# Kernel tuning notes

Measured on AMD Instinct MI355X. Metric: run time of the kernel, lower is better.

Reference implementation:

```python
import jax, jax.numpy as jnp
import numpy as np

BN_EPS = 1e-5

def _batchnorm(h, gamma, beta):
    # PyTorch BatchNorm1d in training mode: biased batch statistics over dim 0
    mu = jnp.mean(h, axis=0)
    var = jnp.mean((h - mu) ** 2, axis=0)
    return (h - mu) * jax.lax.rsqrt(var + BN_EPS) * gamma + beta


def setup_inputs() -> dict:
    key = jax.random.key(0)
    ks = jax.random.split(key, 8)
    N, E, D = 50000, 800000, 128
    x = jax.random.normal(ks[0], (N, D), dtype=jnp.float32)
    edge_index = jax.random.randint(ks[1], (2, E), 0, N, dtype=jnp.int64)
    s1 = 1.0 / np.sqrt(D)
    W1 = jax.random.uniform(ks[2], (D, D), jnp.float32, -s1, s1)
    b1 = jax.random.uniform(ks[3], (D,), jnp.float32, -s1, s1)
    W2 = jax.random.uniform(ks[4], (D, D), jnp.float32, -s1, s1)
    b2 = jax.random.uniform(ks[5], (D,), jnp.float32, -s1, s1)
    g1 = jnp.ones((D,), jnp.float32); beta1 = jnp.zeros((D,), jnp.float32)
    g2 = jnp.ones((D,), jnp.float32); beta2 = jnp.zeros((D,), jnp.float32)
    eps = jnp.array([0.1], jnp.float32)
    return {"x": x, "edge_index": edge_index, "eps": eps,
            "W1": W1, "b1": b1, "g1": g1, "beta1": beta1,
            "W2": W2, "b2": b2, "g2": g2, "beta2": beta2}


def reference(x, edge_index, eps, W1, b1, g1, beta1, W2, b2, g2, beta2):
    src, dst = edge_index[0], edge_index[1]
    N = x.shape[0]
    # gather by src, scatter-add to dst
    aggr = jax.ops.segment_sum(x[src], dst, num_segments=N)
    out = (1.0 + eps) * x + aggr  # eps broadcast (shape [1])
    h = jax.nn.relu(_batchnorm(out @ W1 + b1, g1, beta1))
    h = jax.nn.relu(_batchnorm(h @ W2 + b2, g2, beta2))
    return h
```

## Files before the change

kernel.cpp:

```cpp
#include <hip/hip_runtime.h>

#define D 128
#define FB 4096
#define GCAP 512

typedef __attribute__((ext_vector_type(8))) short short8;
typedef __attribute__((ext_vector_type(4))) float f32x4;

static __device__ __forceinline__ unsigned short f2bf(float f) {
    union { float f; unsigned u; } v; v.f = f;
    unsigned r = v.u + 0x7FFF + ((v.u >> 16) & 1);
    return (unsigned short)(r >> 16);
}

static __device__ __forceinline__ float2 bfpair2f(unsigned p) {
    union { unsigned u; float f; } a, b;
    a.u = (p & 0xFFFFu) << 16;
    b.u = p & 0xFFFF0000u;
    return make_float2(a.f, b.f);
}

__global__ __launch_bounds__(256) void prep_kernel(
    const float4* __restrict__ x4, uint2* __restrict__ xh, int xtotal,
    const float* __restrict__ W1, const float* __restrict__ W2,
    unsigned short* __restrict__ Wf1, unsigned short* __restrict__ Wf2,
    float* __restrict__ stats, int* __restrict__ bucketCount,
    unsigned short* __restrict__ zrow, int xblocks)
{
    if (blockIdx.x < (unsigned)xblocks) {
        int i = blockIdx.x * 256 + threadIdx.x;
        if (i >= xtotal) return;
        float4 v = x4[i];
        uint2 o;
        o.x = (unsigned)f2bf(v.x) | ((unsigned)f2bf(v.y) << 16);
        o.y = (unsigned)f2bf(v.z) | ((unsigned)f2bf(v.w) << 16);
        xh[i] = o;
    } else if (blockIdx.x < (unsigned)(xblocks + 128)) {
        int idx = (blockIdx.x - xblocks) * 256 + threadIdx.x;
        const float* W = (idx < 16384) ? W1 : W2;
        unsigned short* Wf = (idx < 16384) ? Wf1 : Wf2;
        int e = idx & 16383;
        int j = e & 7, lane = (e >> 3) & 63, ckk = e >> 9;
        int ct = ckk & 7, kk = ckk >> 3;
        int k = kk * 32 + (lane >> 4) * 8 + j;
        int n = ct * 16 + (lane & 15);
        Wf[e] = f2bf(W[k * 128 + n]);
    } else {
        int t = threadIdx.x;
        stats[t] = 0.f; stats[t + 256] = 0.f;
        bucketCount[t] = 0; bucketCount[t + 256] = 0;
        if (t < 128) zrow[t] = 0;
    }
}

__global__ __launch_bounds__(256) void bucket_hist_kernel(
    const int* __restrict__ ei, int E, int NB, int* __restrict__ bucketCount)
{
    __shared__ int hist[512];
    int tid = threadIdx.x;
    for (int i = tid; i < NB; i += 256) hist[i] = 0;
    __syncthreads();
    int b0 = blockIdx.x * FB;
    int lim = min(FB, E - b0);
    for (int i = tid; i < lim; i += 256)
        atomicAdd(&hist[ei[E + b0 + i] >> 7], 1);
    __syncthreads();
    for (int i = tid; i < NB; i += 256)
        if (hist[i]) atomicAdd(&bucketCount[i], hist[i]);
}

__global__ __launch_bounds__(512) void bucket_scan_kernel(
    const int* __restrict__ bucketCount, int NB, int E,
    int* __restrict__ bucketBase, int* __restrict__ bucketCursor)
{
    __shared__ int sm[512];
    int tid = threadIdx.x;
    int v = (tid < NB) ? bucketCount[tid] : 0;
    sm[tid] = v;
    __syncthreads();
    #pragma unroll
    for (int off = 1; off < 512; off <<= 1) {
        int u = (tid >= off) ? sm[tid - off] : 0;
        __syncthreads();
        sm[tid] += u;
        __syncthreads();
    }
    if (tid < NB) {
        int ex = sm[tid] - v;
        bucketBase[tid] = ex;
        bucketCursor[tid] = ex;
    }
    if (tid == 0) bucketBase[NB] = E;
}

__global__ __launch_bounds__(256) void bucket_fill_kernel(
    const int* __restrict__ ei, int E, int NB,
    int* __restrict__ bucketCursor, unsigned* __restrict__ rec)
{
    __shared__ int hist[512], base[512];
    int tid = threadIdx.x;
    int b0 = blockIdx.x * FB;
    for (int i = tid; i < NB; i += 256) hist[i] = 0;
    __syncthreads();
    int lim = min(FB, E - b0);
    for (int i = tid; i < lim; i += 256)
        atomicAdd(&hist[ei[E + b0 + i] >> 7], 1);
    __syncthreads();
    for (int i = tid; i < NB; i += 256) {
        int c = hist[i];
        base[i] = c ? atomicAdd(&bucketCursor[i], c) : 0;
        hist[i] = 0;
    }
    __syncthreads();
    for (int i = tid; i < lim; i += 256) {
        int e = b0 + i;
        int dst = ei[E + e], src = ei[e];
        int bk = dst >> 7;
        int r = atomicAdd(&hist[bk], 1);
        rec[base[bk] + r] = ((unsigned)src << 7) | (unsigned)(dst & 127);
    }
}

__global__ __launch_bounds__(256) void bucket_gather_kernel(
    const unsigned* __restrict__ xh, const unsigned* __restrict__ rec,
    const int* __restrict__ bucketBase, const float* __restrict__ epsp,
    unsigned* __restrict__ h0, int N, int zrow)
{
    int bk = blockIdx.x >> 3;
    int sub = blockIdx.x & 7;
    int tid = threadIdx.x;
    int d0 = (bk << 7) + (sub << 4);

    __shared__ int cnts[16], rnk[16], offs[17];
    __shared__ int slist[GCAP];

    if (tid < 16) { cnts[tid] = 0; rnk[tid] = 0; }
    __syncthreads();

    int lo = bucketBase[bk], hi = bucketBase[bk + 1];
    for (int i = lo + tid; i < hi; i += 256) {
        unsigned r = rec[i];
        int dl = r & 127;
        if ((dl >> 4) == sub) atomicAdd(&cnts[dl & 15], 1);
    }
    __syncthreads();
    if (tid == 0) {
        int run = 0;
        #pragma unroll
        for (int i = 0; i < 16; ++i) { offs[i] = run; run += cnts[i]; }
        offs[16] = run;
    }
    __syncthreads();
    for (int i = lo + tid; i < hi; i += 256) {
        unsigned r = rec[i];
        int dl = r & 127;
        if ((dl >> 4) == sub) {
            int d4 = dl & 15;
            int rk = atomicAdd(&rnk[d4], 1);
            int pos = offs[d4] + rk;
            if (pos < GCAP) slist[pos] = (int)(r >> 7);
        }
    }
    __syncthreads();

    int wv = tid >> 6, lane = tid & 63;
    float epsv = 1.0f + __ldg(epsp);

    int dloc = wv * 4;
    int dA = d0 + dloc, dB = dA + 1, dC = dA + 2, dD = dA + 3;
    int vA = (dA < N), vB = (dB < N), vC = (dC < N), vD = (dD < N);

    int iA = offs[dloc + 0], eA = offs[dloc + 1];
    int iB = offs[dloc + 1], eB = offs[dloc + 2];
    int iC = offs[dloc + 2], eC = offs[dloc + 3];
    int iD = offs[dloc + 3], eD = offs[dloc + 4];
    if (iA > GCAP) iA = GCAP;  if (eA > GCAP) eA = GCAP;
    if (iB > GCAP) iB = GCAP;  if (eB > GCAP) eB = GCAP;
    if (iC > GCAP) iC = GCAP;  if (eC > GCAP) eC = GCAP;
    if (iD > GCAP) iD = GCAP;  if (eD > GCAP) eD = GCAP;
    if (!vA) { iA = 0; eA = 0; }
    if (!vB) { iB = 0; eB = 0; }
    if (!vC) { iC = 0; eC = 0; }
    if (!vD) { iD = 0; eD = 0; }

    float2 xvA = bfpair2f(xh[(size_t)(vA ? dA : 0) * 64 + lane]);
    float2 xvB = bfpair2f(xh[(size_t)(vB ? dB : 0) * 64 + lane]);
    float2 xvC = bfpair2f(xh[(size_t)(vC ? dC : 0) * 64 + lane]);
    float2 xvD = bfpair2f(xh[(size_t)(vD ? dD : 0) * 64 + lane]);
    float axA = epsv * xvA.x, ayA = epsv * xvA.y;
    float axB = epsv * xvB.x, ayB = epsv * xvB.y;
    float axC = epsv * xvC.x, ayC = epsv * xvC.y;
    float axD = epsv * xvD.x, ayD = epsv * xvD.y;

    int rA = eA - iA, rB = eB - iB, rC = eC - iC, rD = eD - iD;
    int iters = max(max(rA, rB), max(rC, rD));
    for (int it = 0; it < iters; it += 8) {
        unsigned pA[8], pB[8], pC[8], pD[8];
        #pragma unroll
        for (int k = 0; k < 8; ++k) {
            int idxA = (iA + k < eA) ? slist[iA + k] : zrow;
            int idxB = (iB + k < eB) ? slist[iB + k] : zrow;
            int idxC = (iC + k < eC) ? slist[iC + k] : zrow;
            int idxD = (iD + k < eD) ? slist[iD + k] : zrow;
            pA[k] = xh[(size_t)idxA * 64 + lane];
            pB[k] = xh[(size_t)idxB * 64 + lane];
            pC[k] = xh[(size_t)idxC * 64 + lane];
            pD[k] = xh[(size_t)idxD * 64 + lane];
        }
        #pragma unroll
        for (int k = 0; k < 8; ++k) {
            float2 a = bfpair2f(pA[k]);
            float2 b = bfpair2f(pB[k]);
            float2 c = bfpair2f(pC[k]);
            float2 d = bfpair2f(pD[k]);
            axA += a.x; ayA += a.y;
            axB += b.x; ayB += b.y;
            axC += c.x; ayC += c.y;
            axD += d.x; ayD += d.y;
        }
        iA += 8; iB += 8; iC += 8; iD += 8;
    }
    if (vA) h0[(size_t)dA * 64 + lane] =
        (unsigned)f2bf(axA) | ((unsigned)f2bf(ayA) << 16);
    if (vB) h0[(size_t)dB * 64 + lane] =
        (unsigned)f2bf(axB) | ((unsigned)f2bf(ayB) << 16);
    if (vC) h0[(size_t)dC * 64 + lane] =
        (unsigned)f2bf(axC) | ((unsigned)f2bf(ayC) << 16);
    if (vD) h0[(size_t)dD * 64 + lane] =
        (unsigned)f2bf(axD) | ((unsigned)f2bf(ayD) << 16);
}

static __device__ __forceinline__ short8 bn_relu_pack(
    const unsigned short* arow, int c, const float* scf, const float* shf)
{
    uint4 rw = *(const uint4*)(arow + c);
    float2 p0 = bfpair2f(rw.x), p1 = bfpair2f(rw.y);
    float2 p2 = bfpair2f(rw.z), p3 = bfpair2f(rw.w);
    p0.x = fmaxf(fmaf(p0.x, scf[c + 0], shf[c + 0]), 0.f);
    p0.y = fmaxf(fmaf(p0.y, scf[c + 1], shf[c + 1]), 0.f);
    p1.x = fmaxf(fmaf(p1.x, scf[c + 2], shf[c + 2]), 0.f);
    p1.y = fmaxf(fmaf(p1.y, scf[c + 3], shf[c + 3]), 0.f);
    p2.x = fmaxf(fmaf(p2.x, scf[c + 4], shf[c + 4]), 0.f);
    p2.y = fmaxf(fmaf(p2.y, scf[c + 5], shf[c + 5]), 0.f);
    p3.x = fmaxf(fmaf(p3.x, scf[c + 6], shf[c + 6]), 0.f);
    p3.y = fmaxf(fmaf(p3.y, scf[c + 7], shf[c + 7]), 0.f);
    short8 af;
    af[0] = (short)f2bf(p0.x); af[1] = (short)f2bf(p0.y);
    af[2] = (short)f2bf(p1.x); af[3] = (short)f2bf(p1.y);
    af[4] = (short)f2bf(p2.x); af[5] = (short)f2bf(p2.y);
    af[6] = (short)f2bf(p3.x); af[7] = (short)f2bf(p3.y);
    return af;
}

__global__ __launch_bounds__(256) void gemm_bn_mfma_kernel(
    const unsigned short* __restrict__ a_bf,
    const float* __restrict__ stat_in, const float* __restrict__ gamma,
    const float* __restrict__ beta, float invN,
    const unsigned short* __restrict__ Wf, const float* __restrict__ bias,
    unsigned short* __restrict__ zout,
    float* __restrict__ stat_sum, float* __restrict__ stat_sq,
    int N, int mode)
{
    __shared__ unsigned short Wl[16384];
    __shared__ float part[1024];
    __shared__ float scf[128], shf[128];

    int tid = threadIdx.x;
    {
        float4* dst = (float4*)Wl;
        const float4* srcp = (const float4*)Wf;
        #pragma unroll
        for (int i = 0; i < 8; ++i) dst[tid + i * 256] = srcp[tid + i * 256];
    }
    if (mode == 1 && tid < 128) {
        float mean = stat_in[tid] * invN;
        float var  = stat_in[128 + tid] * invN - mean * mean;
        float sv = gamma[tid] * rsqrtf(var + 1e-5f);
        scf[tid] = sv;
        shf[tid] = fmaf(-mean, sv, beta[tid]);
    }
    __syncthreads();

    int w = tid >> 6, lane = tid & 63, q = lane >> 4, n16 = lane & 15;
    int rowb = blockIdx.x * 128 + w * 16;
    int m0 = rowb + n16;
    int m1 = rowb + 64 + n16;
    int mc0 = (m0 < N) ? m0 : (N - 1);
    int mc1 = (m1 < N) ? m1 : (N - 1);
    const unsigned short* arow0 = a_bf + (size_t)mc0 * D;
    const unsigned short* arow1 = a_bf + (size_t)mc1 * D;

    f32x4 acc0[8], acc1[8];
    #pragma unroll
    for (int ct = 0; ct < 8; ++ct) {
        acc0[ct] = (f32x4){0.f, 0.f, 0.f, 0.f};
        acc1[ct] = (f32x4){0.f, 0.f, 0.f, 0.f};
    }

    #pragma unroll
    for (int kk = 0; kk < 4; ++kk) {
        int c = kk * 32 + q * 8;
        short8 af0, af1;
        if (mode == 0) {
            af0 = *(const short8*)(arow0 + c);
            af1 = *(const short8*)(arow1 + c);
        } else {
            af0 = bn_relu_pack(arow0, c, scf, shf);
            af1 = bn_relu_pack(arow1, c, scf, shf);
        }
        #pragma unroll
        for (int ct = 0; ct < 8; ++ct) {
            short8 bf = *(const short8*)&Wl[(((kk * 8 + ct) * 64) + lane) * 8];
            acc0[ct] = __builtin_amdgcn_mfma_f32_16x16x32_bf16(af0, bf, acc0[ct], 0, 0, 0);
            acc1[ct] = __builtin_amdgcn_mfma_f32_16x16x32_bf16(af1, bf, acc1[ct], 0, 0, 0);
        }
    }

    #pragma unroll
    for (int ct = 0; ct < 8; ++ct) {
        int col = ct * 16 + n16;
        float bv = __ldg(bias + col);
        float s = 0.f, qs = 0.f;
        #pragma unroll
        for (int reg = 0; reg < 4; ++reg) {
            int row = rowb + q * 4 + reg;
            float v = acc0[ct][reg] + bv;
            if (row < N) {
                zout[(size_t)row * D + col] = f2bf(v);
                s += v;
                qs = fmaf(v, v, qs);
            }
        }
        #pragma unroll
        for (int reg = 0; reg < 4; ++reg) {
            int row = rowb + 64 + q * 4 + reg;
            float v = acc1[ct][reg] + bv;
            if (row < N) {
                zout[(size_t)row * D + col] = f2bf(v);
                s += v;
                qs = fmaf(v, v, qs);
            }
        }
        s  += __shfl_xor(s, 16, 64);
        s  += __shfl_xor(s, 32, 64);
        qs += __shfl_xor(qs, 16, 64);
        qs += __shfl_xor(qs, 32, 64);
        if (lane < 16) {
            part[w * 128 + col] = s;
            part[512 + w * 128 + col] = qs;
        }
    }
    __syncthreads();

    if (tid < 128) {
        float s  = part[tid] + part[128 + tid] + part[256 + tid] + part[384 + tid];
        float qq = part[512 + tid] + part[640 + tid] + part[768 + tid] + part[896 + tid];
        atomicAdd(&stat_sum[tid], s);
        atomicAdd(&stat_sq[tid], qq);
    }
}

__global__ __launch_bounds__(256) void bn_relu_kernel(
    const uint2* __restrict__ z2, float4* __restrict__ out,
    const float* __restrict__ stat2, const float* __restrict__ gamma,
    const float* __restrict__ beta, float invN, int total4)
{
    __shared__ float sf[128], tf[128];
    int tid = threadIdx.x;
    if (tid < 128) {
        float mean = stat2[tid] * invN;
        float var  = stat2[128 + tid] * invN - mean * mean;
        float sv = gamma[tid] * rsqrtf(var + 1e-5f);
        sf[tid] = sv;
        tf[tid] = fmaf(-mean, sv, beta[tid]);
    }
    __syncthreads();

    int i = blockIdx.x * 256 + tid;
    if (i >= total4) return;
    uint2 zp = z2[i];
    float2 v01 = bfpair2f(zp.x);
    float2 v23 = bfpair2f(zp.y);
    int c = (i & 31) * 4;
    float4 o;
    o.x = fmaxf(fmaf(v01.x, sf[c + 0], tf[c + 0]), 0.f);
    o.y = fmaxf(fmaf(v01.y, sf[c + 1], tf[c + 1]), 0.f);
    o.z = fmaxf(fmaf(v23.x, sf[c + 2], tf[c + 2]), 0.f);
    o.w = fmaxf(fmaf(v23.y, sf[c + 3], tf[c + 3]), 0.f);
    out[i] = o;
}

extern "C" void kernel_launch(void* const* d_in, const int* in_sizes, int n_in,
                              void* d_out, int out_size, void* d_ws, size_t ws_size,
                              hipStream_t stream)
{
    const float* x   = (const float*)d_in[0];
    const int*   ei  = (const int*)d_in[1];
    const float* eps = (const float*)d_in[2];
    const float* W1  = (const float*)d_in[3];
    const float* b1  = (const float*)d_in[4];
    const float* g1  = (const float*)d_in[5];
    const float* be1 = (const float*)d_in[6];
    const float* W2  = (const float*)d_in[7];
    const float* b2  = (const float*)d_in[8];
    const float* g2  = (const float*)d_in[9];
    const float* be2 = (const float*)d_in[10];

    int N = in_sizes[0] / D;
    int E = in_sizes[1] / 2;
    size_t ND = (size_t)N * D;
    int NB = (N + 127) >> 7;

    unsigned short* xh  = (unsigned short*)d_ws;
    unsigned short* z1  = xh;
    unsigned short* region2 = xh + ND + 128;
    unsigned* rec       = (unsigned*)region2;
    unsigned short* z2  = region2;
    float* stats        = (float*)(region2 + ND);
    int* bucketCount    = (int*)(stats + 512);
    int* bucketBase     = bucketCount + 512;
    int* bucketCursor   = bucketBase + 513;
    unsigned short* Wf1 = (unsigned short*)(bucketCursor + 512);
    unsigned short* Wf2 = Wf1 + 16384;

    float* sum1 = stats + 0,   *sq1 = stats + 128;
    float* sum2 = stats + 256, *sq2 = stats + 384;
    unsigned short* h0 = (unsigned short*)d_out;

    int xtotal = N * 32;
    int xblocks = (xtotal + 255) / 256;
    prep_kernel<<<xblocks + 129, 256, 0, stream>>>(
        (const float4*)x, (uint2*)xh, xtotal, W1, W2, Wf1, Wf2,
        stats, bucketCount, xh + ND, xblocks);

    int fblocks = (E + FB - 1) / FB;
    bucket_hist_kernel<<<fblocks, 256, 0, stream>>>(ei, E, NB, bucketCount);
    bucket_scan_kernel<<<1, 512, 0, stream>>>(bucketCount, NB, E, bucketBase, bucketCursor);
    bucket_fill_kernel<<<fblocks, 256, 0, stream>>>(ei, E, NB, bucketCursor, rec);
    bucket_gather_kernel<<<NB * 8, 256, 0, stream>>>(
        (const unsigned*)xh, rec, bucketBase, eps, (unsigned*)h0, N, N);

    int gblocks = (N + 127) / 128;
    gemm_bn_mfma_kernel<<<gblocks, 256, 0, stream>>>(
        h0, nullptr, nullptr, nullptr, 0.f,
        Wf1, b1, z1, sum1, sq1, N, 0);
    gemm_bn_mfma_kernel<<<gblocks, 256, 0, stream>>>(
        z1, sum1, g1, be1, 1.0f / N,
        Wf2, b2, z2, sum2, sq2, N, 1);
    bn_relu_kernel<<<(N * 32 + 255) / 256, 256, 0, stream>>>(
        (const uint2*)z2, (float4*)d_out, sum2, g2, be2, 1.0f / N, N * 32);
}
```

Before: 222.9 us.

## Bucket edges per 16 destinations and gather rows with half-wave uint2 loads

Shrinks the edge bucket granularity from 128 to 16 destination nodes. Each gather block now reads only its own bucket, where before eight sub-blocks each rescanned a 128-node bucket. The scan becomes a two-level per-thread scan so it can cover up to 3328 buckets. The gather pads each node's source list to multiples of 8 with a zero-row sentinel and has the two wave halves load different edges as 8-byte chunks, combining them with a cross-half shuffle. In exchange the bucket histogram and fill kernels use larger shared arrays, which may lower their occupancy.

Result: slower. 229.5 us (+3.0%).

```diff
diff --git a/kernel.cpp b/kernel.cpp
--- a/kernel.cpp
+++ b/kernel.cpp
@@ -1,8 +1,10 @@
 #include <hip/hip_runtime.h>
 
 #define D 128
-#define FB 4096
+#define FB2 8192
 #define GCAP 512
+#define NBMAX 3328
+#define SCAN_PER 13
 
 typedef __attribute__((ext_vector_type(8))) short short8;
 typedef __attribute__((ext_vector_type(4))) float f32x4;
@@ -18,6 +20,35 @@
     a.u = (p & 0xFFFFu) << 16;
     b.u = p & 0xFFFF0000u;
     return make_float2(a.f, b.f);
+}
+
+static __device__ __forceinline__ void acc2(f32x4& A, uint2 p) {
+    union { unsigned u; float f; } t;
+    float f0, f1, f2, f3;
+    t.u = p.x << 16;          f0 = t.f;
+    t.u = p.x & 0xFFFF0000u;  f1 = t.f;
+    t.u = p.y << 16;          f2 = t.f;
+    t.u = p.y & 0xFFFF0000u;  f3 = t.f;
+    A[0] += f0; A[1] += f1; A[2] += f2; A[3] += f3;
+}
+
+static __device__ __forceinline__ void emit_row(
+    unsigned* h0, int d, unsigned lane8, float epsv, uint2 xv, f32x4 A)
+{
+    union { unsigned u; float f; } t;
+    float x0, x1, x2, x3;
+    t.u = xv.x << 16;          x0 = t.f;
+    t.u = xv.x & 0xFFFF0000u;  x1 = t.f;
+    t.u = xv.y << 16;          x2 = t.f;
+    t.u = xv.y & 0xFFFF0000u;  x3 = t.f;
+    float r0 = fmaf(epsv, x0, A[0]);
+    float r1 = fmaf(epsv, x1, A[1]);
+    float r2 = fmaf(epsv, x2, A[2]);
+    float r3 = fmaf(epsv, x3, A[3]);
+    uint2 o;
+    o.x = (unsigned)f2bf(r0) | ((unsigned)f2bf(r1) << 16);
+    o.y = (unsigned)f2bf(r2) | ((unsigned)f2bf(r3) << 16);
+    *(uint2*)((char*)h0 + ((unsigned)(d * 256) + lane8)) = o;
 }
 
 __global__ __launch_bounds__(256) void prep_kernel(
@@ -48,65 +79,78 @@
     } else {
         int t = threadIdx.x;
         stats[t] = 0.f; stats[t + 256] = 0.f;
-        bucketCount[t] = 0; bucketCount[t + 256] = 0;
+        for (int i = t; i < NBMAX; i += 256) bucketCount[i] = 0;
         if (t < 128) zrow[t] = 0;
     }
 }
 
 __global__ __launch_bounds__(256) void bucket_hist_kernel(
-    const int* __restrict__ ei, int E, int NB, int* __restrict__ bucketCount)
-{
-    __shared__ int hist[512];
-    int tid = threadIdx.x;
-    for (int i = tid; i < NB; i += 256) hist[i] = 0;
-    __syncthreads();
-    int b0 = blockIdx.x * FB;
-    int lim = min(FB, E - b0);
+    const int* __restrict__ ei, int E, int NB2, int* __restrict__ bucketCount)
+{
+    __shared__ int hist[NBMAX];
+    int tid = threadIdx.x;
+    for (int i = tid; i < NB2; i += 256) hist[i] = 0;
+    __syncthreads();
+    int b0 = blockIdx.x * FB2;
+    int lim = min(FB2, E - b0);
     for (int i = tid; i < lim; i += 256)
-        atomicAdd(&hist[ei[E + b0 + i] >> 7], 1);
-    __syncthreads();
-    for (int i = tid; i < NB; i += 256)
+        atomicAdd(&hist[ei[E + b0 + i] >> 4], 1);
+    __syncthreads();
+    for (int i = tid; i < NB2; i += 256)
         if (hist[i]) atomicAdd(&bucketCount[i], hist[i]);
 }
 
-__global__ __launch_bounds__(512) void bucket_scan_kernel(
-    const int* __restrict__ bucketCount, int NB, int E,
+__global__ __launch_bounds__(256) void bucket_scan_kernel(
+    const int* __restrict__ bucketCount, int NB2, int E,
     int* __restrict__ bucketBase, int* __restrict__ bucketCursor)
 {
-    __shared__ int sm[512];
-    int tid = threadIdx.x;
-    int v = (tid < NB) ? bucketCount[tid] : 0;
-    sm[tid] = v;
-    __syncthreads();
-    #pragma unroll
-    for (int off = 1; off < 512; off <<= 1) {
-        int u = (tid >= off) ? sm[tid - off] : 0;
+    __shared__ int part[256];
+    int tid = threadIdx.x;
+    int loc[SCAN_PER];
+    int s = 0;
+    #pragma unroll
+    for (int j = 0; j < SCAN_PER; ++j) {
+        int idx = tid * SCAN_PER + j;
+        int v = (idx < NB2) ? bucketCount[idx] : 0;
+        loc[j] = s;
+        s += v;
+    }
+    part[tid] = s;
+    __syncthreads();
+    #pragma unroll
+    for (int off = 1; off < 256; off <<= 1) {
+        int u = (tid >= off) ? part[tid - off] : 0;
         __syncthreads();
-        sm[tid] += u;
+        part[tid] += u;
         __syncthreads();
     }
-    if (tid < NB) {
-        int ex = sm[tid] - v;
-        bucketBase[tid] = ex;
-        bucketCursor[tid] = ex;
-    }
-    if (tid == 0) bucketBase[NB] = E;
+    int tb = (tid > 0) ? part[tid - 1] : 0;
+    #pragma unroll
+    for (int j = 0; j < SCAN_PER; ++j) {
+        int idx = tid * SCAN_PER + j;
+        if (idx < NB2) {
+            int ex = tb + loc[j];
+            bucketBase[idx] = ex;
+            bucketCursor[idx] = ex;
+        }
+    }
+    if (tid == 0) bucketBase[NB2] = E;
 }
 
 __global__ __launch_bounds__(256) void bucket_fill_kernel(
-    const int* __restrict__ ei, int E, int NB,
+    const int* __restrict__ ei, int E, int NB2,
     int* __restrict__ bucketCursor, unsigned* __restrict__ rec)
 {
-    __shared__ int hist[512], base[512];
-    int tid = threadIdx.x;
-    int b0 = blockIdx.x * FB;
-    for (int i = tid; i < NB; i += 256) hist[i] = 0;
-    __syncthreads();
-    int lim = min(FB, E - b0);
+    __shared__ int hist[NBMAX], base[NBMAX];
+    int tid = threadIdx.x;
+    int b0 = blockIdx.x * FB2;
+    for (int i = tid; i < NB2; i += 256) hist[i] = 0;
+    __syncthreads();
+    int lim = min(FB2, E - b0);
     for (int i = tid; i < lim; i += 256)
-        atomicAdd(&hist[ei[E + b0 + i] >> 7], 1);
-    __syncthreads();
-    for (int i = tid; i < NB; i += 256) {
+        atomicAdd(&hist[ei[E + b0 + i] >> 4], 1);
+    __syncthreads();
+    for (int i = tid; i < NB2; i += 256) {
         int c = hist[i];
         base[i] = c ? atomicAdd(&bucketCursor[i], c) : 0;
         hist[i] = 0;
@@ -115,119 +159,116 @@
     for (int i = tid; i < lim; i += 256) {
         int e = b0 + i;
         int dst = ei[E + e], src = ei[e];
-        int bk = dst >> 7;
+        int bk = dst >> 4;
         int r = atomicAdd(&hist[bk], 1);
-        rec[base[bk] + r] = ((unsigned)src << 7) | (unsigned)(dst & 127);
+        rec[base[bk] + r] = ((unsigned)src << 4) | (unsigned)(dst & 15);
     }
 }
 
 __global__ __launch_bounds__(256) void bucket_gather_kernel(
     const unsigned* __restrict__ xh, const unsigned* __restrict__ rec,
     const int* __restrict__ bucketBase, const float* __restrict__ epsp,
-    unsigned* __restrict__ h0, int N, int zrow)
-{
-    int bk = blockIdx.x >> 3;
-    int sub = blockIdx.x & 7;
-    int tid = threadIdx.x;
-    int d0 = (bk << 7) + (sub << 4);
+    unsigned* __restrict__ h0, int N, int zoff)
+{
+    int g = blockIdx.x;
+    int tid = threadIdx.x;
+    int d0 = g << 4;
 
     __shared__ int cnts[16], rnk[16], offs[17];
-    __shared__ int slist[GCAP];
+    __shared__ int slist[GCAP + 8];
 
     if (tid < 16) { cnts[tid] = 0; rnk[tid] = 0; }
-    __syncthreads();
-
-    int lo = bucketBase[bk], hi = bucketBase[bk + 1];
+    for (int i = tid; i < GCAP + 8; i += 256) slist[i] = zoff;
+    __syncthreads();
+
+    int lo = bucketBase[g], hi = bucketBase[g + 1];
+    for (int i = lo + tid; i < hi; i += 256)
+        atomicAdd(&cnts[rec[i] & 15], 1);
+    __syncthreads();
+    if (tid == 0) {
+        int run = 0;
+        #pragma unroll
+        for (int i = 0; i < 16; ++i) {
+            offs[i] = run;
+            run += (cnts[i] + 7) & ~7;
+            if (run > GCAP) run = GCAP;
+        }
+        offs[16] = run;
+    }
+    __syncthreads();
     for (int i = lo + tid; i < hi; i += 256) {
         unsigned r = rec[i];
-        int dl = r & 127;
-        if ((dl >> 4) == sub) atomicAdd(&cnts[dl & 15], 1);
-    }
-    __syncthreads();
-    if (tid == 0) {
-        int run = 0;
-        #pragma unroll
-        for (int i = 0; i < 16; ++i) { offs[i] = run; run += cnts[i]; }
-        offs[16] = run;
-    }
-    __syncthreads();
-    for (int i = lo + tid; i < hi; i += 256) {
-        unsigned r = rec[i];
-        int dl = r & 127;
-        if ((dl >> 4) == sub) {
-            int d4 = dl & 15;
-            int rk = atomicAdd(&rnk[d4], 1);
-            int pos = offs[d4] + rk;
-            if (pos < GCAP) slist[pos] = (int)(r >> 7);
-        }
+        int d = r & 15;
+        int rk = atomicAdd(&rnk[d], 1);
+        int pos = offs[d] + rk;
+        if (pos < offs[d + 1]) slist[pos] = (int)((r >> 4) << 8);
     }
     __syncthreads();
 
     int wv = tid >> 6, lane = tid & 63;
+    int half = lane >> 5, l5 = lane & 31;
+    unsigned lane8 = (unsigned)(l5 << 3);
     float epsv = 1.0f + __ldg(epsp);
+    const char* xc = (const char*)xh;
 
     int dloc = wv * 4;
     int dA = d0 + dloc, dB = dA + 1, dC = dA + 2, dD = dA + 3;
     int vA = (dA < N), vB = (dB < N), vC = (dC < N), vD = (dD < N);
 
-    int iA = offs[dloc + 0], eA = offs[dloc + 1];
-    int iB = offs[dloc + 1], eB = offs[dloc + 2];
-    int iC = offs[dloc + 2], eC = offs[dloc + 3];
-    int iD = offs[dloc + 3], eD = offs[dloc + 4];
-    if (iA > GCAP) iA = GCAP;  if (eA > GCAP) eA = GCAP;
-    if (iB > GCAP) iB = GCAP;  if (eB > GCAP) eB = GCAP;
-    if (iC > GCAP) iC = GCAP;  if (eC > GCAP) eC = GCAP;
-    if (iD > GCAP) iD = GCAP;  if (eD > GCAP) eD = GCAP;
-    if (!vA) { iA = 0; eA = 0; }
-    if (!vB) { iB = 0; eB = 0; }
-    if (!vC) { iC = 0; eC = 0; }
-    if (!vD) { iD = 0; eD = 0; }
-
-    float2 xvA = bfpair2f(xh[(size_t)(vA ? dA : 0) * 64 + lane]);
-    float2 xvB = bfpair2f(xh[(size_t)(vB ? dB : 0) * 64 + lane]);
-    float2 xvC = bfpair2f(xh[(size_t)(vC ? dC : 0) * 64 + lane]);
-    float2 xvD = bfpair2f(xh[(size_t)(vD ? dD : 0) * 64 + lane]);
-    float axA = epsv * xvA.x, ayA = epsv * xvA.y;
-    float axB = epsv * xvB.x, ayB = epsv * xvB.y;
-    float axC = epsv * xvC.x, ayC = epsv * xvC.y;
-    float axD = epsv * xvD.x, ayD = epsv * xvD.y;
-
-    int rA = eA - iA, rB = eB - iB, rC = eC - iC, rD = eD - iD;
-    int iters = max(max(rA, rB), max(rC, rD));
-    for (int it = 0; it < iters; it += 8) {
-        unsigned pA[8], pB[8], pC[8], pD[8];
-        #pragma unroll
-        for (int k = 0; k < 8; ++k) {
-            int idxA = (iA + k < eA) ? slist[iA + k] : zrow;
-            int idxB = (iB + k < eB) ? slist[iB + k] : zrow;
-            int idxC = (iC + k < eC) ? slist[iC + k] : zrow;
-            int idxD = (iD + k < eD) ? slist[iD + k] : zrow;
-            pA[k] = xh[(size_t)idxA * 64 + lane];
-            pB[k] = xh[(size_t)idxB * 64 + lane];
-            pC[k] = xh[(size_t)idxC * 64 + lane];
-            pD[k] = xh[(size_t)idxD * 64 + lane];
-        }
-        #pragma unroll
-        for (int k = 0; k < 8; ++k) {
-            float2 a = bfpair2f(pA[k]);
-            float2 b = bfpair2f(pB[k]);
-            float2 c = bfpair2f(pC[k]);
-            float2 d = bfpair2f(pD[k]);
-            axA += a.x; ayA += a.y;
-            axB += b.x; ayB += b.y;
-            axC += c.x; ayC += c.y;
-            axD += d.x; ayD += d.y;
-        }
-        iA += 8; iB += 8; iC += 8; iD += 8;
-    }
-    if (vA) h0[(size_t)dA * 64 + lane] =
-        (unsigned)f2bf(axA) | ((unsigned)f2bf(ayA) << 16);
-    if (vB) h0[(size_t)dB * 64 + lane] =
-        (unsigned)f2bf(axB) | ((unsigned)f2bf(ayB) << 16);
-    if (vC) h0[(size_t)dC * 64 + lane] =
-        (unsigned)f2bf(axC) | ((unsigned)f2bf(ayC) << 16);
-    if (vD) h0[(size_t)dD * 64 + lane] =
-        (unsigned)f2bf(axD) | ((unsigned)f2bf(ayD) << 16);
+    int s0 = offs[dloc + 0], s1 = offs[dloc + 1];
+    int s2 = offs[dloc + 2], s3 = offs[dloc + 3], s4 = offs[dloc + 4];
+    int nch0 = (s1 - s0) >> 3, nch1 = (s2 - s1) >> 3;
+    int nch2 = (s3 - s2) >> 3, nch3 = (s4 - s3) >> 3;
+    int iters = max(max(nch0, nch1), max(nch2, nch3));
+
+    uint2 xv0 = *(const uint2*)(xc + (unsigned)((vA ? dA : 0) * 256) + lane8);
+    uint2 xv1 = *(const uint2*)(xc + (unsigned)((vB ? dB : 0) * 256) + lane8);
+    uint2 xv2 = *(const uint2*)(xc + (unsigned)((vC ? dC : 0) * 256) + lane8);
+    uint2 xv3 = *(const uint2*)(xc + (unsigned)((vD ? dD : 0) * 256) + lane8);
+
+    f32x4 A0 = (f32x4){0.f, 0.f, 0.f, 0.f};
+    f32x4 A1 = (f32x4){0.f, 0.f, 0.f, 0.f};
+    f32x4 A2 = (f32x4){0.f, 0.f, 0.f, 0.f};
+    f32x4 A3 = (f32x4){0.f, 0.f, 0.f, 0.f};
+
+    for (int c = 0; c < iters; ++c) {
+        int b0 = (c < nch0) ? (s0 + (c << 3)) : GCAP;
+        int b1 = (c < nch1) ? (s1 + (c << 3)) : GCAP;
+        int b2 = (c < nch2) ? (s2 + (c << 3)) : GCAP;
+        int b3 = (c < nch3) ? (s3 + (c << 3)) : GCAP;
+        uint2 p0[4], p1[4], p2[4], p3[4];
+        #pragma unroll
+        for (int k = 0; k < 4; ++k) {
+            unsigned o0 = (unsigned)slist[b0 + 2 * k + half];
+            unsigned o1 = (unsigned)slist[b1 + 2 * k + half];
+            unsigned o2 = (unsigned)slist[b2 + 2 * k + half];
+            unsigned o3 = (unsigned)slist[b3 + 2 * k + half];
+            p0[k] = *(const uint2*)(xc + (o0 + lane8));
+            p1[k] = *(const uint2*)(xc + (o1 + lane8));
+            p2[k] = *(const uint2*)(xc + (o2 + lane8));
+            p3[k] = *(const uint2*)(xc + (o3 + lane8));
+        }
+        #pragma unroll
+        for (int k = 0; k < 4; ++k) {
+            acc2(A0, p0[k]); acc2(A1, p1[k]);
+            acc2(A2, p2[k]); acc2(A3, p3[k]);
+        }
+    }
+
+    #pragma unroll
+    for (int r = 0; r < 4; ++r) {
+        A0[r] += __shfl_xor(A0[r], 32, 64);
+        A1[r] += __shfl_xor(A1[r], 32, 64);
+        A2[r] += __shfl_xor(A2[r], 32, 64);
+        A3[r] += __shfl_xor(A3[r], 32, 64);
+    }
+
+    if (half == 0) {
+        if (vA) emit_row(h0, dA, lane8, epsv, xv0, A0);
+        if (vB) emit_row(h0, dB, lane8, epsv, xv1, A1);
+        if (vC) emit_row(h0, dC, lane8, epsv, xv2, A2);
+        if (vD) emit_row(h0, dD, lane8, epsv, xv3, A3);
+    }
 }
 
 static __device__ __forceinline__ short8 bn_relu_pack(
@@ -409,18 +450,18 @@
     int N = in_sizes[0] / D;
     int E = in_sizes[1] / 2;
     size_t ND = (size_t)N * D;
-    int NB = (N + 127) >> 7;
+    int NB2 = (N + 15) >> 4;
 
     unsigned short* xh  = (unsigned short*)d_ws;
     unsigned short* z1  = xh;
     unsigned short* region2 = xh + ND + 128;
     unsigned* rec       = (unsigned*)region2;
     unsigned short* z2  = region2;
+    int* bucketCount    = (int*)((char*)region2 + (4 << 20));
+    int* bucketBase     = bucketCount + NBMAX;
+    int* bucketCursor   = bucketBase + NBMAX + 1;
     float* stats        = (float*)(region2 + ND);
-    int* bucketCount    = (int*)(stats + 512);
-    int* bucketBase     = bucketCount + 512;
-    int* bucketCursor   = bucketBase + 513;
-    unsigned short* Wf1 = (unsigned short*)(bucketCursor + 512);
+    unsigned short* Wf1 = (unsigned short*)(stats + 512);
     unsigned short* Wf2 = Wf1 + 16384;
 
     float* sum1 = stats + 0,   *sq1 = stats + 128;
@@ -433,12 +474,12 @@
         (const float4*)x, (uint2*)xh, xtotal, W1, W2, Wf1, Wf2,
         stats, bucketCount, xh + ND, xblocks);
 
-    int fblocks = (E + FB - 1) / FB;
-    bucket_hist_kernel<<<fblocks, 256, 0, stream>>>(ei, E, NB, bucketCount);
-    bucket_scan_kernel<<<1, 512, 0, stream>>>(bucketCount, NB, E, bucketBase, bucketCursor);
-    bucket_fill_kernel<<<fblocks, 256, 0, stream>>>(ei, E, NB, bucketCursor, rec);
-    bucket_gather_kernel<<<NB * 8, 256, 0, stream>>>(
-        (const unsigned*)xh, rec, bucketBase, eps, (unsigned*)h0, N, N);
+    int fblocks = (E + FB2 - 1) / FB2;
+    bucket_hist_kernel<<<fblocks, 256, 0, stream>>>(ei, E, NB2, bucketCount);
+    bucket_scan_kernel<<<1, 256, 0, stream>>>(bucketCount, NB2, E, bucketBase, bucketCursor);
+    bucket_fill_kernel<<<fblocks, 256, 0, stream>>>(ei, E, NB2, bucketCursor, rec);
+    bucket_gather_kernel<<<NB2, 256, 0, stream>>>(
+        (const unsigned*)xh, rec, bucketBase, eps, (unsigned*)h0, N, N * 256);
 
     int gblocks = (N + 127) / 128;
     gemm_bn_mfma_kernel<<<gblocks, 256, 0, stream>>>(
```
